# Performance work log

Hardware: AMD Instinct MI355X
Metric: run time of the kernel (lower is better)

## Reference

```python
import jax, jax.numpy as jnp
import numpy as np
from jax import lax

B, C, T, H, HEAD, NC = 256, 64, 2048, 64, 32, 8

def setup_inputs() -> dict:
    key = jax.random.key(0)
    ks = jax.random.split(key, 20)
    s = 0.08
    d = {}
    d["x"] = jax.random.normal(ks[0], (B, C, T), jnp.float32)
    # GRU layer 0: input C -> hidden H (gates order r,z,n as in PyTorch)
    d["w_ih0"] = jax.random.normal(ks[1], (3 * H, C), jnp.float32) * s
    d["w_hh0"] = jax.random.normal(ks[2], (3 * H, H), jnp.float32) * s
    d["b_ih0"] = jax.random.normal(ks[3], (3 * H,), jnp.float32) * s
    d["b_hh0"] = jax.random.normal(ks[4], (3 * H,), jnp.float32) * s
    # GRU layer 1: H -> H
    d["w_ih1"] = jax.random.normal(ks[5], (3 * H, H), jnp.float32) * s
    d["w_hh1"] = jax.random.normal(ks[6], (3 * H, H), jnp.float32) * s
    d["b_ih1"] = jax.random.normal(ks[7], (3 * H,), jnp.float32) * s
    d["b_hh1"] = jax.random.normal(ks[8], (3 * H,), jnp.float32) * s
    # additive attention: Linear(H,H) -> tanh -> Linear(H,1)
    d["attn_w1"] = jax.random.normal(ks[9], (H, H), jnp.float32) * s
    d["attn_b1"] = jax.random.normal(ks[10], (H,), jnp.float32) * s
    d["attn_w2"] = jax.random.normal(ks[11], (1, H), jnp.float32) * s
    d["attn_b2"] = jax.random.normal(ks[12], (1,), jnp.float32) * s
    # head: LayerNorm(H) -> Linear(H,32) -> GELU -> Linear(32,NC)
    d["ln_g"] = jnp.ones((H,), jnp.float32)
    d["ln_b"] = jnp.zeros((H,), jnp.float32)
    d["head_w1"] = jax.random.normal(ks[13], (HEAD, H), jnp.float32) * s
    d["head_b1"] = jax.random.normal(ks[14], (HEAD,), jnp.float32) * s
    d["head_w2"] = jax.random.normal(ks[15], (NC, HEAD), jnp.float32) * s
    d["head_b2"] = jax.random.normal(ks[16], (NC,), jnp.float32) * s
    return d


def _gru_layer(x, w_ih, w_hh, b_ih, b_hh):
    # x: (B, T, F) -> (B, T, H). PyTorch GRU cell math, gate order r,z,n.
    bsz = x.shape[0]
    hid = w_hh.shape[1]
    # precompute input contributions for all timesteps in one big GEMM
    xg = jnp.einsum('btf,gf->btg', x, w_ih) + b_ih  # (B, T, 3H)
    xg = jnp.swapaxes(xg, 0, 1)  # (T, B, 3H)

    def step(h, xg_t):
        hg = h @ w_hh.T + b_hh  # (B, 3H)
        xr, xz, xn = jnp.split(xg_t, 3, axis=-1)
        hr, hz, hn = jnp.split(hg, 3, axis=-1)
        r = jax.nn.sigmoid(xr + hr)
        z = jax.nn.sigmoid(xz + hz)
        n = jnp.tanh(xn + r * hn)
        h_new = (1.0 - z) * n + z * h
        return h_new, h_new

    h0 = jnp.zeros((bsz, hid), x.dtype)
    _, hs = lax.scan(step, h0, xg)  # hs: (T, B, H)
    return jnp.swapaxes(hs, 0, 1)


def _forward(x, w_ih0, w_hh0, b_ih0, b_hh0, w_ih1, w_hh1, b_ih1, b_hh1,
             attn_w1, attn_b1, attn_w2, attn_b2, ln_g, ln_b,
             head_w1, head_b1, head_w2, head_b2):
    xt = jnp.swapaxes(x, 1, 2)  # (B, T, C)
    h = _gru_layer(xt, w_ih0, w_hh0, b_ih0, b_hh0)
    h = _gru_layer(h, w_ih1, w_hh1, b_ih1, b_hh1)  # (B, T, H)
    # additive attention pooling
    a = jnp.tanh(jnp.einsum('bth,oh->bto', h, attn_w1) + attn_b1)
    w = jnp.einsum('bth,oh->bto', a, attn_w2)[..., 0] + attn_b2[0]  # (B, T)
    w = jax.nn.softmax(w, axis=-1)
    pooled = jnp.einsum('bth,bt->bh', h, w)  # (B, H)
    # LayerNorm (eps=1e-5 as in torch)
    mu = jnp.mean(pooled, axis=-1, keepdims=True)
    var = jnp.mean(jnp.square(pooled - mu), axis=-1, keepdims=True)
    y = (pooled - mu) * lax.rsqrt(var + 1e-5) * ln_g + ln_b
    y = jax.nn.gelu(y @ head_w1.T + head_b1, approximate=False)
    return y @ head_w2.T + head_b2  # (B, NC)


def reference(x, w_ih0, w_hh0, b_ih0, b_hh0, w_ih1, w_hh1, b_ih1, b_hh1,
              attn_w1, attn_b1, attn_w2, attn_b2, ln_g, ln_b,
              head_w1, head_b1, head_w2, head_b2):
    return _forward(x, w_ih0, w_hh0, b_ih0, b_hh0, w_ih1, w_hh1, b_ih1, b_hh1,
                    attn_w1, attn_b1, attn_w2, attn_b2, ln_g, ln_b,
                    head_w1, head_b1, head_w2, head_b2)
```

## Files before the change

kernel.cpp:

```cpp
#include <hip/hip_runtime.h>
#include <math.h>

#define TS 2048

typedef float f32x2 __attribute__((ext_vector_type(2)));
typedef _Float16 f16;
typedef _Float16 f16x2 __attribute__((ext_vector_type(2)));
typedef _Float16 f16x8 __attribute__((ext_vector_type(8)));

#define XG0_B  5120
#define XG1_B  8192
#define H0H_B  11264
#define H1H_B  12288
#define H1F_B  12800
#define SCRO_B 13824
#define LDSF   13920

#define BAR() do { asm volatile("s_waitcnt lgkmcnt(0)" ::: "memory"); __builtin_amdgcn_s_barrier(); } while(0)
#define FEN() asm volatile("s_waitcnt lgkmcnt(0)" ::: "memory")

union H8 { f16x8 v8; f16x2 v2[4]; };

__device__ __forceinline__ float sigmoidf_(float v){ return __builtin_amdgcn_rcpf(1.0f+__expf(-v)); }
__device__ __forceinline__ float tanhf_(float v){
  v = fminf(15.0f, fmaxf(-15.0f, v));
  const float e = __expf(2.0f*v);
  return (e-1.0f)*__builtin_amdgcn_rcpf(e+1.0f);
}
__device__ __forceinline__ float qadd1(float v){
  return v + __int_as_float(__builtin_amdgcn_update_dpp(0, __float_as_int(v), 0xB1, 0xF, 0xF, true));
}
__device__ __forceinline__ float wsum64(float v){
  v += __int_as_float(__builtin_amdgcn_update_dpp(0, __float_as_int(v), 0x111, 0xF, 0xF, true));
  v += __int_as_float(__builtin_amdgcn_update_dpp(0, __float_as_int(v), 0x112, 0xF, 0xF, true));
  v += __int_as_float(__builtin_amdgcn_update_dpp(0, __float_as_int(v), 0x114, 0xF, 0xF, true));
  v += __int_as_float(__builtin_amdgcn_update_dpp(0, __float_as_int(v), 0x118, 0xF, 0xF, true));
  v += __int_as_float(__builtin_amdgcn_update_dpp(0, __float_as_int(v), 0x142, 0xA, 0xF, true));
  v += __int_as_float(__builtin_amdgcn_update_dpp(0, __float_as_int(v), 0x143, 0xC, 0xF, true));
  return __int_as_float(__builtin_amdgcn_readlane(__float_as_int(v), 63));
}
__device__ __forceinline__ float fdot2_(f16x2 a, f16x2 b, float c){
  return __builtin_amdgcn_fdot2(a, b, c, false);
}
__device__ __forceinline__ void dot6(const f16* vec, const f16x2* Wp,
                                     float& a00, float& a01, float& a02,
                                     float& a10, float& a11, float& a12){
  H8 u[4];
  u[0].v8 = *(const f16x8*)(vec);
  u[1].v8 = *(const f16x8*)(vec+8);
  u[2].v8 = *(const f16x8*)(vec+16);
  u[3].v8 = *(const f16x8*)(vec+24);
  #pragma unroll
  for (int m=0;m<16;m++){
    const f16x2 hm = u[m>>2].v2[m&3];
    a00 = fdot2_(Wp[m],    hm, a00);
    a01 = fdot2_(Wp[16+m], hm, a01);
    a02 = fdot2_(Wp[32+m], hm, a02);
    a10 = fdot2_(Wp[48+m], hm, a10);
    a11 = fdot2_(Wp[64+m], hm, a11);
    a12 = fdot2_(Wp[80+m], hm, a12);
  }
}

__global__ __launch_bounds__(448, 1)
void gru_attn_fused(const float* __restrict__ x,
                    const float* __restrict__ w_ih0, const float* __restrict__ w_hh0,
                    const float* __restrict__ b_ih0, const float* __restrict__ b_hh0,
                    const float* __restrict__ w_ih1, const float* __restrict__ w_hh1,
                    const float* __restrict__ b_ih1, const float* __restrict__ b_hh1,
                    const float* __restrict__ attn_w1, const float* __restrict__ attn_b1,
                    const float* __restrict__ attn_w2, const float* __restrict__ attn_b2,
                    const float* __restrict__ ln_g, const float* __restrict__ ln_b,
                    const float* __restrict__ head_w1, const float* __restrict__ head_b1,
                    const float* __restrict__ head_w2, const float* __restrict__ head_b2,
                    float* __restrict__ out)
{
  __shared__ float lds[LDSF];
  f16*   ldsx = (f16*)lds;
  float* xg0  = lds + XG0_B;
  float* xg1  = lds + XG1_B;
  f16*   h0h  = (f16*)(lds + H0H_B);
  f16*   h1h  = (f16*)(lds + H1H_B);
  float* h1f  = lds + H1F_B;

  const int tid  = threadIdx.x;
  const int wid  = tid >> 6;
  const int lane = tid & 63;
  const int b    = blockIdx.x;
  const float* xb = x + (size_t)b * 64 * TS;

  const int i2     = lane >> 1;
  const int p      = lane & 1;
  const int ownrow = i2 + 32*p;
  const int hoff   = p << 5;

  f16x2 W[96];
  float4 SP[16];
  float bA=0.f,bB=0.f,bC=0.f,w2o=0.f,b2v=0.f;

  if (wid < 4) {
    const float* wsrc = (wid==0)? w_hh0 : (wid==1)? w_hh1 : (wid==2)? w_ih1 : w_ih0;
    for (int r2=0;r2<2;r2++)
      for (int g=0;g<3;g++)
        for (int m=0;m<16;m++){
          const f32x2 v = *(const f32x2*)(wsrc + (size_t)(g*64 + i2 + 32*r2)*64 + hoff + 2*m);
          W[(r2*3+g)*16+m] = (f16x2){(f16)v.x,(f16)v.y};
        }
    for (int q2=0;q2<96;q2++) asm volatile("" : "+v"(W[q2]));
    const float* bsrc = (wid==0)? b_hh0 : (wid==1)? b_hh1 : (wid==2)? b_ih1 : b_ih0;
    bA = bsrc[ownrow]; bB = bsrc[64+ownrow]; bC = bsrc[128+ownrow];
  } else if (wid == 6) {
    for (int r2=0;r2<2;r2++)
      for (int m=0;m<16;m++){
        const f32x2 v = *(const f32x2*)(attn_w1 + (size_t)(i2+32*r2)*64 + hoff + 2*m);
        W[r2*16+m] = (f16x2){(f16)v.x,(f16)v.y};
      }
    for (int q2=0;q2<32;q2++) asm volatile("" : "+v"(W[q2]));
    bA = attn_b1[ownrow]; w2o = attn_w2[ownrow]; b2v = attn_b2[0];
  }

  for (int idx = tid; idx < 1024; idx += 448) ((uint32_t*)h0h)[idx] = 0u;
  for (int idx = tid; idx < 512;  idx += 448) ((uint32_t*)h1h)[idx] = 0u;
  if (wid == 4) {
    const float* src = xb + (size_t)lane*TS;
    #pragma unroll
    for (int kq=0;kq<16;kq++) SP[kq] = *(const float4*)(src + 4*kq);
    #pragma unroll
    for (int kq=0;kq<16;kq++){
      ldsx[(4*kq+0)*80 + lane] = (f16)SP[kq].x;
      ldsx[(4*kq+1)*80 + lane] = (f16)SP[kq].y;
      ldsx[(4*kq+2)*80 + lane] = (f16)SP[kq].z;
      ldsx[(4*kq+3)*80 + lane] = (f16)SP[kq].w;
    }
  }
  __syncthreads();

  if (wid <= 1) __builtin_amdgcn_s_setprio(1);

  float hreg = 0.f;
  float am = -1e30f, aZ = 0.f, aP = 0.f;

  #pragma unroll 1
  for (int k = -1; k <= 258; ++k) {
    if (wid <= 1) {
      const int blk = k - (wid << 1);
      if (0 <= blk && blk < 256) {
        f16*   hring = wid ? h1h : h0h;
        float* xgc   = wid ? xg1 : xg0;
        const int emask = wid ? 1023 : 2047;
        #pragma unroll
        for (int j=0;j<8;j++){
          const int t  = (blk<<3) + j;
          const int xi = (t & 15) * 192;
          const float xgr = xgc[xi + ownrow];
          const float xgz = xgc[xi + 64 + ownrow];
          const float xgn = xgc[xi + 128 + ownrow];
          FEN();
          const f16* hv = hring + (((t-1)<<6) & emask) + hoff;
          float a00=0,a01=0,a02=0,a10=0,a11=0,a12=0;
          dot6(hv, W, a00,a01,a02,a10,a11,a12);
          a00=qadd1(a00); a01=qadd1(a01); a02=qadd1(a02);
          a10=qadd1(a10); a11=qadd1(a11); a12=qadd1(a12);
          const float hr = p ? a10 : a00;
          const float hz = p ? a11 : a01;
          const float hn = p ? a12 : a02;
          const float r = sigmoidf_(xgr + hr + bA);
          const float z = sigmoidf_(xgz + hz + bB);
          const float n = tanhf_(xgn + r*(hn + bC));
          hreg = n + z*(hreg - n);
          hring[((t<<6) & emask) + ownrow] = (f16)hreg;
          if (wid) h1f[((t&15)<<6) + ownrow] = hreg;
        }
      }
    } else if (wid <= 3) {
      const int blk = (wid==2) ? k-1 : k+1;
      if (0 <= blk && blk < 256) {
        float* xgw = (wid==2) ? xg1 : xg0;
        #pragma unroll
        for (int j=0;j<8;j++){
          const int t = (blk<<3) + j;
          const f16* vec;
          if (wid==2) vec = h0h + (((t-1)<<6) & 2047) + hoff;
          else        vec = ldsx + ((t>>6)&1)*5120 + (t&63)*80 + hoff;
          float a00=0,a01=0,a02=0,a10=0,a11=0,a12=0;
          dot6(vec, W, a00,a01,a02,a10,a11,a12);
          a00=qadd1(a00); a01=qadd1(a01); a02=qadd1(a02);
          a10=qadd1(a10); a11=qadd1(a11); a12=qadd1(a12);
          const int xi = (t & 15) * 192;
          xgw[xi + ownrow]       = (p ? a10 : a00) + bA;
          xgw[xi + 64 + ownrow]  = (p ? a11 : a01) + bB;
          xgw[xi + 128 + ownrow] = (p ? a12 : a02) + bC;
        }
      }
    } else if (wid == 4) {
      const int kk = k + 1, tile = kk >> 3, ph = kk & 7;
      if (ph == 1 && tile < 31) {
        const float* src = xb + (size_t)lane*TS + (tile+1)*64;
        #pragma unroll
        for (int kq=0;kq<16;kq++) SP[kq] = *(const float4*)(src + 4*kq);
      } else if (ph == 5 && tile < 31) {
        f16* dsth = ldsx + ((tile+1)&1)*5120;
        #pragma unroll
        for (int kq=0;kq<16;kq++){
          dsth[(4*kq+0)*80 + lane] = (f16)SP[kq].x;
          dsth[(4*kq+1)*80 + lane] = (f16)SP[kq].y;
          dsth[(4*kq+2)*80 + lane] = (f16)SP[kq].z;
          dsth[(4*kq+3)*80 + lane] = (f16)SP[kq].w;
        }
      }
    } else if (wid == 6) {
      const int blk = k - 3;
      if (0 <= blk && blk < 256) {
        #pragma unroll
        for (int j=0;j<8;j++){
          const int t = (blk<<3) + j;
          const f16* hv = h1h + ((t&15)<<6) + hoff;
          H8 u[4];
          u[0].v8 = *(const f16x8*)(hv);
          u[1].v8 = *(const f16x8*)(hv+8);
          u[2].v8 = *(const f16x8*)(hv+16);
          u[3].v8 = *(const f16x8*)(hv+24);
          float a0=0.f, a1=0.f;
          #pragma unroll
          for (int m=0;m<16;m++){
            const f16x2 hm = u[m>>2].v2[m&3];
            a0 = fdot2_(W[m],    hm, a0);
            a1 = fdot2_(W[16+m], hm, a1);
          }
          a0 = qadd1(a0); a1 = qadd1(a1);
          const float a  = tanhf_((p ? a1 : a0) + bA);
          const float s  = wsum64(w2o * a) + b2v;
          const float hc = h1f[((t&15)<<6) + lane];
          const float mn = fmaxf(am, s);
          const float sc = __expf(am - mn);
          const float pp = __expf(s - mn);
          aZ = aZ*sc + pp;
          aP = aP*sc + pp*hc;
          am = mn;
        }
      }
    }
    BAR();
  }

  if (wid == 6) {
    const float pooled = aP / aZ;
    float mu = pooled;
    #pragma unroll
    for (int m=1;m<64;m<<=1) mu += __shfl_xor(mu, m, 64);
    mu *= (1.0f/64.0f);
    const float d = pooled - mu;
    float var = d*d;
    #pragma unroll
    for (int m=1;m<64;m<<=1) var += __shfl_xor(var, m, 64);
    var *= (1.0f/64.0f);
    const float y = d * rsqrtf(var + 1e-5f) * ln_g[lane] + ln_b[lane];
    lds[SCRO_B + lane] = y;
  }
  __syncthreads();
  if (tid < 32) {
    const float* hw = head_w1 + tid*64;
    float acc = head_b1[tid];
    #pragma unroll
    for (int kq=0;kq<16;kq++){
      const float4 w4 = ((const float4*)hw)[kq];
      acc += w4.x*lds[SCRO_B+4*kq+0] + w4.y*lds[SCRO_B+4*kq+1]
           + w4.z*lds[SCRO_B+4*kq+2] + w4.w*lds[SCRO_B+4*kq+3];
    }
    const float u = 0.5f*acc*(1.0f + erff(acc*0.70710678118654752f));
    lds[SCRO_B + 64 + tid] = u;
  }
  __syncthreads();
  if (tid < 8) {
    const float* hw = head_w2 + tid*32;
    float acc = head_b2[tid];
    #pragma unroll
    for (int kq=0;kq<8;kq++){
      const float4 w4 = ((const float4*)hw)[kq];
      acc += w4.x*lds[SCRO_B+64+4*kq+0] + w4.y*lds[SCRO_B+64+4*kq+1]
           + w4.z*lds[SCRO_B+64+4*kq+2] + w4.w*lds[SCRO_B+64+4*kq+3];
    }
    out[b*8 + tid] = acc;
  }
}

extern "C" void kernel_launch(void* const* d_in, const int* in_sizes, int n_in,
                              void* d_out, int out_size, void* d_ws, size_t ws_size,
                              hipStream_t stream) {
  (void)in_sizes; (void)n_in; (void)d_ws; (void)ws_size; (void)out_size;
  const float* x       = (const float*)d_in[0];
  const float* w_ih0   = (const float*)d_in[1];
  const float* w_hh0   = (const float*)d_in[2];
  const float* b_ih0   = (const float*)d_in[3];
  const float* b_hh0   = (const float*)d_in[4];
  const float* w_ih1   = (const float*)d_in[5];
  const float* w_hh1   = (const float*)d_in[6];
  const float* b_ih1   = (const float*)d_in[7];
  const float* b_hh1   = (const float*)d_in[8];
  const float* attn_w1 = (const float*)d_in[9];
  const float* attn_b1 = (const float*)d_in[10];
  const float* attn_w2 = (const float*)d_in[11];
  const float* attn_b2 = (const float*)d_in[12];
  const float* ln_g    = (const float*)d_in[13];
  const float* ln_b    = (const float*)d_in[14];
  const float* head_w1 = (const float*)d_in[15];
  const float* head_b1 = (const float*)d_in[16];
  const float* head_w2 = (const float*)d_in[17];
  const float* head_b2 = (const float*)d_in[18];
  hipLaunchKernelGGL(gru_attn_fused, dim3(256), dim3(448), 0, stream,
                     x, w_ih0, w_hh0, b_ih0, b_hh0, w_ih1, w_hh1, b_ih1, b_hh1,
                     attn_w1, attn_b1, attn_w2, attn_b2, ln_g, ln_b,
                     head_w1, head_b1, head_w2, head_b2, (float*)d_out);
}
```

Before: 792.3 us.

## Process two batch elements per block with interleaved recurrences and fp16 gate buffers

Each workgroup now handles two batch elements, so the grid shrinks from 256 to 128 blocks. Every wave runs two independent GRU and attention chains back to back inside each step, which lets one chain's latency hide behind the other's work. The input-gate buffers and the layer-1 hidden copy move to fp16 so both elements fit in LDS, the x staging tile shrinks to 32 timesteps, and the explicit LDS fence before the recurrent dot is dropped. The risks are a longer serial critical path per block, fewer active CUs on a 256-CU part, and lower precision in the stored gate pre-activations.

```diff
diff --git a/kernel.cpp b/kernel.cpp
--- a/kernel.cpp
+++ b/kernel.cpp
@@ -8,16 +8,14 @@
 typedef _Float16 f16x2 __attribute__((ext_vector_type(2)));
 typedef _Float16 f16x8 __attribute__((ext_vector_type(8)));
 
-#define XG0_B  5120
-#define XG1_B  8192
-#define H0H_B  11264
-#define H1H_B  12288
-#define H1F_B  12800
+#define XG0_B  4608
+#define XG1_B  7680
+#define H0H_B  10752
+#define H1H_B  12800
 #define SCRO_B 13824
-#define LDSF   13920
+#define LDSF   14016
 
 #define BAR() do { asm volatile("s_waitcnt lgkmcnt(0)" ::: "memory"); __builtin_amdgcn_s_barrier(); } while(0)
-#define FEN() asm volatile("s_waitcnt lgkmcnt(0)" ::: "memory")
 
 union H8 { f16x8 v8; f16x2 v2[4]; };
 
@@ -76,26 +74,26 @@
                     float* __restrict__ out)
 {
   __shared__ float lds[LDSF];
-  f16*   ldsx = (f16*)lds;
-  float* xg0  = lds + XG0_B;
-  float* xg1  = lds + XG1_B;
-  f16*   h0h  = (f16*)(lds + H0H_B);
-  f16*   h1h  = (f16*)(lds + H1H_B);
-  float* h1f  = lds + H1F_B;
+  f16* ldsx = (f16*)lds;
+  f16* xg0h = (f16*)(lds + XG0_B);
+  f16* xg1h = (f16*)(lds + XG1_B);
+  f16* h0h  = (f16*)(lds + H0H_B);
+  f16* h1h  = (f16*)(lds + H1H_B);
 
   const int tid  = threadIdx.x;
   const int wid  = tid >> 6;
   const int lane = tid & 63;
-  const int b    = blockIdx.x;
-  const float* xb = x + (size_t)b * 64 * TS;
-
+  const int blkx = blockIdx.x;
   const int i2     = lane >> 1;
   const int p      = lane & 1;
   const int ownrow = i2 + 32*p;
   const int hoff   = p << 5;
+  const size_t xstr = (size_t)64 * TS;
+  const float* xb0 = x + (size_t)(2*blkx) * xstr;
+  const float* xb1 = xb0 + xstr;
 
   f16x2 W[96];
-  float4 SP[16];
+  float4 SP[2][8];
   float bA=0.f,bB=0.f,bC=0.f,w2o=0.f,b2v=0.f;
 
   if (wid < 4) {
@@ -119,124 +117,152 @@
     bA = attn_b1[ownrow]; w2o = attn_w2[ownrow]; b2v = attn_b2[0];
   }
 
-  for (int idx = tid; idx < 1024; idx += 448) ((uint32_t*)h0h)[idx] = 0u;
-  for (int idx = tid; idx < 512;  idx += 448) ((uint32_t*)h1h)[idx] = 0u;
+  for (int idx = tid; idx < 3072; idx += 448) ((uint32_t*)(lds + H0H_B))[idx] = 0u;
   if (wid == 4) {
-    const float* src = xb + (size_t)lane*TS;
-    #pragma unroll
-    for (int kq=0;kq<16;kq++) SP[kq] = *(const float4*)(src + 4*kq);
-    #pragma unroll
-    for (int kq=0;kq<16;kq++){
-      ldsx[(4*kq+0)*80 + lane] = (f16)SP[kq].x;
-      ldsx[(4*kq+1)*80 + lane] = (f16)SP[kq].y;
-      ldsx[(4*kq+2)*80 + lane] = (f16)SP[kq].z;
-      ldsx[(4*kq+3)*80 + lane] = (f16)SP[kq].w;
+    #pragma unroll
+    for (int be=0;be<2;be++){
+      const float* src = (be ? xb1 : xb0) + (size_t)lane*TS;
+      #pragma unroll
+      for (int q=0;q<8;q++) SP[be][q] = *(const float4*)(src + 4*q);
+    }
+    #pragma unroll
+    for (int be=0;be<2;be++){
+      f16* dst = ldsx + be*4608;
+      #pragma unroll
+      for (int q=0;q<8;q++){
+        dst[(4*q+0)*72 + lane] = (f16)SP[be][q].x;
+        dst[(4*q+1)*72 + lane] = (f16)SP[be][q].y;
+        dst[(4*q+2)*72 + lane] = (f16)SP[be][q].z;
+        dst[(4*q+3)*72 + lane] = (f16)SP[be][q].w;
+      }
     }
   }
   __syncthreads();
 
   if (wid <= 1) __builtin_amdgcn_s_setprio(1);
 
-  float hreg = 0.f;
-  float am = -1e30f, aZ = 0.f, aP = 0.f;
+  float hreg0=0.f, hreg1=0.f;
+  float am0=-1e30f, aZ0=0.f, aP0=0.f;
+  float am1=-1e30f, aZ1=0.f, aP1=0.f;
 
   #pragma unroll 1
   for (int k = -1; k <= 258; ++k) {
     if (wid <= 1) {
-      const int blk = k - (wid << 1);
-      if (0 <= blk && blk < 256) {
-        f16*   hring = wid ? h1h : h0h;
-        float* xgc   = wid ? xg1 : xg0;
+      const int blkk = k - (wid << 1);
+      if (0 <= blkk && blkk < 256) {
+        f16* hring = wid ? h1h : h0h;
+        f16* xgc   = wid ? xg1h : xg0h;
         const int emask = wid ? 1023 : 2047;
+        const int bstr  = wid ? 1024 : 2048;
         #pragma unroll
         for (int j=0;j<8;j++){
-          const int t  = (blk<<3) + j;
-          const int xi = (t & 15) * 192;
-          const float xgr = xgc[xi + ownrow];
-          const float xgz = xgc[xi + 64 + ownrow];
-          const float xgn = xgc[xi + 128 + ownrow];
-          FEN();
-          const f16* hv = hring + (((t-1)<<6) & emask) + hoff;
-          float a00=0,a01=0,a02=0,a10=0,a11=0,a12=0;
-          dot6(hv, W, a00,a01,a02,a10,a11,a12);
-          a00=qadd1(a00); a01=qadd1(a01); a02=qadd1(a02);
-          a10=qadd1(a10); a11=qadd1(a11); a12=qadd1(a12);
-          const float hr = p ? a10 : a00;
-          const float hz = p ? a11 : a01;
-          const float hn = p ? a12 : a02;
-          const float r = sigmoidf_(xgr + hr + bA);
-          const float z = sigmoidf_(xgz + hz + bB);
-          const float n = tanhf_(xgn + r*(hn + bC));
-          hreg = n + z*(hreg - n);
-          hring[((t<<6) & emask) + ownrow] = (f16)hreg;
-          if (wid) h1f[((t&15)<<6) + ownrow] = hreg;
+          const int t = (blkk<<3) + j;
+          #pragma unroll
+          for (int be=0;be<2;be++){
+            const int xi = be*3072 + (t&15)*192;
+            const float xgr = (float)xgc[xi + ownrow];
+            const float xgz = (float)xgc[xi + 64 + ownrow];
+            const float xgn = (float)xgc[xi + 128 + ownrow];
+            const f16* hv = hring + be*bstr + (((t-1)<<6) & emask) + hoff;
+            float a00=0,a01=0,a02=0,a10=0,a11=0,a12=0;
+            dot6(hv, W, a00,a01,a02,a10,a11,a12);
+            a00=qadd1(a00); a01=qadd1(a01); a02=qadd1(a02);
+            a10=qadd1(a10); a11=qadd1(a11); a12=qadd1(a12);
+            const float hr = p ? a10 : a00;
+            const float hz = p ? a11 : a01;
+            const float hn = p ? a12 : a02;
+            const float r = sigmoidf_(xgr + hr + bA);
+            const float z = sigmoidf_(xgz + hz + bB);
+            const float n = tanhf_(xgn + r*(hn + bC));
+            float h = be ? hreg1 : hreg0;
+            h = n + z*(h - n);
+            if (be) hreg1 = h; else hreg0 = h;
+            hring[be*bstr + ((t<<6) & emask) + ownrow] = (f16)h;
+          }
         }
       }
     } else if (wid <= 3) {
-      const int blk = (wid==2) ? k-1 : k+1;
-      if (0 <= blk && blk < 256) {
-        float* xgw = (wid==2) ? xg1 : xg0;
+      const int blkk = (wid==2) ? k-1 : k+1;
+      if (0 <= blkk && blkk < 256) {
+        f16* xgw = (wid==2) ? xg1h : xg0h;
         #pragma unroll
         for (int j=0;j<8;j++){
-          const int t = (blk<<3) + j;
-          const f16* vec;
-          if (wid==2) vec = h0h + (((t-1)<<6) & 2047) + hoff;
-          else        vec = ldsx + ((t>>6)&1)*5120 + (t&63)*80 + hoff;
-          float a00=0,a01=0,a02=0,a10=0,a11=0,a12=0;
-          dot6(vec, W, a00,a01,a02,a10,a11,a12);
-          a00=qadd1(a00); a01=qadd1(a01); a02=qadd1(a02);
-          a10=qadd1(a10); a11=qadd1(a11); a12=qadd1(a12);
-          const int xi = (t & 15) * 192;
-          xgw[xi + ownrow]       = (p ? a10 : a00) + bA;
-          xgw[xi + 64 + ownrow]  = (p ? a11 : a01) + bB;
-          xgw[xi + 128 + ownrow] = (p ? a12 : a02) + bC;
+          const int t = (blkk<<3) + j;
+          #pragma unroll
+          for (int be=0;be<2;be++){
+            const f16* vec;
+            if (wid==2) vec = h0h + be*2048 + (((t-1)<<6) & 2047) + hoff;
+            else        vec = ldsx + be*4608 + ((t>>5)&1)*2304 + (t&31)*72 + hoff;
+            float a00=0,a01=0,a02=0,a10=0,a11=0,a12=0;
+            dot6(vec, W, a00,a01,a02,a10,a11,a12);
+            a00=qadd1(a00); a01=qadd1(a01); a02=qadd1(a02);
+            a10=qadd1(a10); a11=qadd1(a11); a12=qadd1(a12);
+            const float gr = (p ? a10 : a00) + bA;
+            const float gz = (p ? a11 : a01) + bB;
+            const float gn = (p ? a12 : a02) + bC;
+            const int xi = be*3072 + (t&15)*192;
+            xgw[xi + ownrow]       = (f16)gr;
+            xgw[xi + 64 + ownrow]  = (f16)gz;
+            xgw[xi + 128 + ownrow] = (f16)gn;
+          }
         }
       }
     } else if (wid == 4) {
-      const int kk = k + 1, tile = kk >> 3, ph = kk & 7;
-      if (ph == 1 && tile < 31) {
-        const float* src = xb + (size_t)lane*TS + (tile+1)*64;
-        #pragma unroll
-        for (int kq=0;kq<16;kq++) SP[kq] = *(const float4*)(src + 4*kq);
-      } else if (ph == 5 && tile < 31) {
-        f16* dsth = ldsx + ((tile+1)&1)*5120;
-        #pragma unroll
-        for (int kq=0;kq<16;kq++){
-          dsth[(4*kq+0)*80 + lane] = (f16)SP[kq].x;
-          dsth[(4*kq+1)*80 + lane] = (f16)SP[kq].y;
-          dsth[(4*kq+2)*80 + lane] = (f16)SP[kq].z;
-          dsth[(4*kq+3)*80 + lane] = (f16)SP[kq].w;
+      const int kk = k + 1, ph = kk & 3, Q = (kk >> 2) + 1;
+      if (Q <= 63) {
+        if (ph == 1) {
+          #pragma unroll
+          for (int be=0;be<2;be++){
+            const float* src = (be ? xb1 : xb0) + (size_t)lane*TS + Q*32;
+            #pragma unroll
+            for (int q=0;q<8;q++) SP[be][q] = *(const float4*)(src + 4*q);
+          }
+        } else if (ph == 3) {
+          #pragma unroll
+          for (int be=0;be<2;be++){
+            f16* dst = ldsx + be*4608 + (Q&1)*2304;
+            #pragma unroll
+            for (int q=0;q<8;q++){
+              dst[(4*q+0)*72 + lane] = (f16)SP[be][q].x;
+              dst[(4*q+1)*72 + lane] = (f16)SP[be][q].y;
+              dst[(4*q+2)*72 + lane] = (f16)SP[be][q].z;
+              dst[(4*q+3)*72 + lane] = (f16)SP[be][q].w;
+            }
+          }
         }
       }
     } else if (wid == 6) {
-      const int blk = k - 3;
-      if (0 <= blk && blk < 256) {
+      const int blkk = k - 3;
+      if (0 <= blkk && blkk < 256) {
         #pragma unroll
         for (int j=0;j<8;j++){
-          const int t = (blk<<3) + j;
-          const f16* hv = h1h + ((t&15)<<6) + hoff;
-          H8 u[4];
-          u[0].v8 = *(const f16x8*)(hv);
-          u[1].v8 = *(const f16x8*)(hv+8);
-          u[2].v8 = *(const f16x8*)(hv+16);
-          u[3].v8 = *(const f16x8*)(hv+24);
-          float a0=0.f, a1=0.f;
-          #pragma unroll
-          for (int m=0;m<16;m++){
-            const f16x2 hm = u[m>>2].v2[m&3];
-            a0 = fdot2_(W[m],    hm, a0);
-            a1 = fdot2_(W[16+m], hm, a1);
-          }
-          a0 = qadd1(a0); a1 = qadd1(a1);
-          const float a  = tanhf_((p ? a1 : a0) + bA);
-          const float s  = wsum64(w2o * a) + b2v;
-          const float hc = h1f[((t&15)<<6) + lane];
-          const float mn = fmaxf(am, s);
-          const float sc = __expf(am - mn);
-          const float pp = __expf(s - mn);
-          aZ = aZ*sc + pp;
-          aP = aP*sc + pp*hc;
-          am = mn;
+          const int t = (blkk<<3) + j;
+          #pragma unroll
+          for (int be=0;be<2;be++){
+            const f16* hv = h1h + be*1024 + ((t&15)<<6) + hoff;
+            H8 u[4];
+            u[0].v8 = *(const f16x8*)(hv);
+            u[1].v8 = *(const f16x8*)(hv+8);
+            u[2].v8 = *(const f16x8*)(hv+16);
+            u[3].v8 = *(const f16x8*)(hv+24);
+            float a0=0.f, a1=0.f;
+            #pragma unroll
+            for (int m=0;m<16;m++){
+              const f16x2 hm = u[m>>2].v2[m&3];
+              a0 = fdot2_(W[m],    hm, a0);
+              a1 = fdot2_(W[16+m], hm, a1);
+            }
+            a0 = qadd1(a0); a1 = qadd1(a1);
+            const float a  = tanhf_((p ? a1 : a0) + bA);
+            const float s  = wsum64(w2o * a) + b2v;
+            const float hc = (float)h1h[be*1024 + ((t&15)<<6) + lane];
+            const float mo = be ? am1 : am0;
+            const float mn = fmaxf(mo, s);
+            const float sc = __expf(mo - mn);
+            const float pp = __expf(s - mn);
+            if (be) { aZ1 = aZ1*sc + pp; aP1 = aP1*sc + pp*hc; am1 = mn; }
+            else    { aZ0 = aZ0*sc + pp; aP0 = aP0*sc + pp*hc; am0 = mn; }
+          }
         }
       }
     }
@@ -244,43 +270,48 @@
   }
 
   if (wid == 6) {
-    const float pooled = aP / aZ;
-    float mu = pooled;
-    #pragma unroll
-    for (int m=1;m<64;m<<=1) mu += __shfl_xor(mu, m, 64);
-    mu *= (1.0f/64.0f);
-    const float d = pooled - mu;
-    float var = d*d;
-    #pragma unroll
-    for (int m=1;m<64;m<<=1) var += __shfl_xor(var, m, 64);
-    var *= (1.0f/64.0f);
-    const float y = d * rsqrtf(var + 1e-5f) * ln_g[lane] + ln_b[lane];
-    lds[SCRO_B + lane] = y;
+    #pragma unroll
+    for (int be=0;be<2;be++){
+      const float pooled = (be ? aP1/aZ1 : aP0/aZ0);
+      float mu = pooled;
+      #pragma unroll
+      for (int m=1;m<64;m<<=1) mu += __shfl_xor(mu, m, 64);
+      mu *= (1.0f/64.0f);
+      const float d = pooled - mu;
+      float var = d*d;
+      #pragma unroll
+      for (int m=1;m<64;m<<=1) var += __shfl_xor(var, m, 64);
+      var *= (1.0f/64.0f);
+      const float y = d * rsqrtf(var + 1e-5f) * ln_g[lane] + ln_b[lane];
+      lds[SCRO_B + be*96 + lane] = y;
+    }
   }
   __syncthreads();
-  if (tid < 32) {
-    const float* hw = head_w1 + tid*64;
-    float acc = head_b1[tid];
+  if (wid <= 1 && lane < 32) {
+    const int be = wid;
+    const float* hw = head_w1 + lane*64;
+    float acc = head_b1[lane];
     #pragma unroll
     for (int kq=0;kq<16;kq++){
       const float4 w4 = ((const float4*)hw)[kq];
-      acc += w4.x*lds[SCRO_B+4*kq+0] + w4.y*lds[SCRO_B+4*kq+1]
-           + w4.z*lds[SCRO_B+4*kq+2] + w4.w*lds[SCRO_B+4*kq+3];
+      acc += w4.x*lds[SCRO_B+be*96+4*kq+0] + w4.y*lds[SCRO_B+be*96+4*kq+1]
+           + w4.z*lds[SCRO_B+be*96+4*kq+2] + w4.w*lds[SCRO_B+be*96+4*kq+3];
     }
     const float u = 0.5f*acc*(1.0f + erff(acc*0.70710678118654752f));
-    lds[SCRO_B + 64 + tid] = u;
+    lds[SCRO_B + be*96 + 64 + lane] = u;
   }
   __syncthreads();
-  if (tid < 8) {
-    const float* hw = head_w2 + tid*32;
-    float acc = head_b2[tid];
+  if (wid <= 1 && lane < 8) {
+    const int be = wid;
+    const float* hw = head_w2 + lane*32;
+    float acc = head_b2[lane];
     #pragma unroll
     for (int kq=0;kq<8;kq++){
       const float4 w4 = ((const float4*)hw)[kq];
-      acc += w4.x*lds[SCRO_B+64+4*kq+0] + w4.y*lds[SCRO_B+64+4*kq+1]
-           + w4.z*lds[SCRO_B+64+4*kq+2] + w4.w*lds[SCRO_B+64+4*kq+3];
-    }
-    out[b*8 + tid] = acc;
+      acc += w4.x*lds[SCRO_B+be*96+64+4*kq+0] + w4.y*lds[SCRO_B+be*96+64+4*kq+1]
+           + w4.z*lds[SCRO_B+be*96+64+4*kq+2] + w4.w*lds[SCRO_B+be*96+64+4*kq+3];
+    }
+    out[(size_t)(2*blkx + be)*8 + lane] = acc;
   }
 }
 
@@ -307,7 +338,7 @@
   const float* head_b1 = (const float*)d_in[16];
   const float* head_w2 = (const float*)d_in[17];
   const float* head_b2 = (const float*)d_in[18];
-  hipLaunchKernelGGL(gru_attn_fused, dim3(256), dim3(448), 0, stream,
+  hipLaunchKernelGGL(gru_attn_fused, dim3(128), dim3(448), 0, stream,
                      x, w_ih0, w_hh0, b_ih0, b_hh0, w_ih1, w_hh1, b_ih1, b_hh1,
                      attn_w1, attn_b1, attn_w2, attn_b2, ln_g, ln_b,
                      head_w1, head_b1, head_w2, head_b2, (float*)d_out);
```

Result: slower. 1.569 ms (+98.0%).
